# Kernel optimization log

Measured on AMD Instinct MI355X. Metric: run time of the kernel, lower is better.

## Reference

```python
import jax, jax.numpy as jnp
import numpy as np

N_QUBITS = 4
DIM = 2 ** N_QUBITS  # 16
N_PATCH = 14 * 14    # 196 patches of 2x2 on a 28x28 image
NUM_CLASSES = 10


def setup_inputs() -> dict:
    key = jax.random.key(0)
    kx, kw, kb, ku = jax.random.split(key, 4)
    B = 8192
    x = jax.random.uniform(kx, (B, 1, 28, 28), dtype=jnp.float32)
    # RandomLayer (8 random 2-qubit gates) composed into one fixed 16x16 real
    # orthogonal unitary (real because RY encoding + real-parameter gates).
    rng = np.random.default_rng(0)
    A = rng.standard_normal((DIM, DIM)).astype(np.float32)
    Q, _ = np.linalg.qr(A)
    U = jnp.asarray(Q, dtype=jnp.float32)
    W = jax.random.normal(kw, (NUM_CLASSES, N_PATCH * N_QUBITS), dtype=jnp.float32) * 0.02
    b = jax.random.normal(kb, (NUM_CLASSES,), dtype=jnp.float32) * 0.02
    return {"x": x, "U": U, "W": W, "b": b}


def _quanv_features(x, U):
    B = x.shape[0]
    # extract 2x2 patches in row-major order: data = [x[r,c], x[r,c+1], x[r+1,c], x[r+1,c+1]]
    p = x.reshape(B, 14, 2, 14, 2).transpose(0, 1, 3, 2, 4).reshape(B, N_PATCH, 4)
    half = 0.5 * p
    a = jnp.stack([jnp.cos(half), jnp.sin(half)], axis=-1)  # (B,P,4,2): RY(theta)|0>
    # product state over 4 qubits -> statevector (B,P,16), wire 0 = most significant
    state = jnp.einsum('bpi,bpj,bpk,bpl->bpijkl',
                       a[:, :, 0], a[:, :, 1], a[:, :, 2], a[:, :, 3]).reshape(B, N_PATCH, DIM)
    state = jnp.einsum('bpd,ed->bpe', state, U)  # apply random-layer unitary
    probs = state * state                          # (B,P,16), real amplitudes
    # PauliZ expectation per wire: sign (+1/-1) of each qubit bit in basis index
    bits = (jnp.arange(DIM)[:, None] >> jnp.arange(N_QUBITS - 1, -1, -1)[None, :]) & 1
    zsign = (1.0 - 2.0 * bits).astype(jnp.float32)  # (16,4)
    meas = probs @ zsign                             # (B,P,4)
    return meas.reshape(B, N_PATCH * N_QUBITS)       # patch-major, qubit-minor (matches torch.cat)


def reference(x, U, W, b):
    feat = _quanv_features(x, U)
    logits = feat @ W.T + b
    return jax.nn.log_softmax(logits, axis=-1)
```

## Files before the change

### kernel.cpp

```cpp
#include <hip/hip_runtime.h>

typedef __attribute__((ext_vector_type(8))) short short8;
typedef __attribute__((ext_vector_type(4))) float f32x4;

#define THREADS 256
#define WPB 4
#define N_PATCH 196
#define NCLS 10
#define FEAT 784
#define ROWSH 24

union I4S8 { int i[4]; short8 v; };

__global__ __launch_bounds__(THREADS, 4)
void quanv_mfma_kernel(const float* __restrict__ x,
                       const float* __restrict__ U,
                       const float* __restrict__ W,
                       const float* __restrict__ b,
                       float* __restrict__ out, int n_img)
{
    __shared__ unsigned short sB[WPB][2][64][ROWSH];

    const int t    = threadIdx.x;
    const int w    = t >> 6;
    const int lane = t & 63;
    const int img  = blockIdx.x * WPB + w;
    if (img >= n_img) return;

    const int colc = lane & 15;
    const int kb   = lane >> 4;
    const float sgn0 = (kb & 2) ? -1.f : 1.f;
    const float sgn1 = (kb & 1) ? -1.f : 1.f;

    short8 a1, a2;
    {
        const float* Urow = U + colc * 16 + (kb & 1) * 8;
        unsigned ub[8]; float uf[8];
#pragma unroll
        for (int i = 0; i < 8; ++i) { uf[i] = Urow[i]; ub[i] = __float_as_uint(uf[i]); }
        I4S8 hi, lo;
#pragma unroll
        for (int j = 0; j < 4; ++j)
            hi.i[j] = (int)__builtin_amdgcn_perm(ub[2*j+1], ub[2*j], 0x07060302u);
#pragma unroll
        for (int j = 0; j < 4; ++j) {
            unsigned lb0 = __float_as_uint(uf[2*j]   - __uint_as_float(ub[2*j]   & 0xffff0000u));
            unsigned lb1 = __float_as_uint(uf[2*j+1] - __uint_as_float(ub[2*j+1] & 0xffff0000u));
            lo.i[j] = (kb < 2) ? (int)__builtin_amdgcn_perm(lb1, lb0, 0x07060302u) : 0;
        }
        a1 = hi.v; a2 = lo.v;
    }

    const float* ximg = x + (size_t)img * FEAT;

    float acc[NCLS];
#pragma unroll
    for (int c = 0; c < NCLS; ++c) acc[c] = 0.f;

#pragma unroll 1
    for (int it = 0; it < 4; ++it) {
        asm volatile("s_waitcnt lgkmcnt(0)" ::: "memory");

        const int pm    = it * 64 + lane;
        const bool vld  = (pm < N_PATCH);
        const int  pc   = vld ? pm : N_PATCH - 1;
        const int  r    = pc / 14;
        const int  cl   = pc - r * 14;
        const float* px = ximg + r * 56 + cl * 2;
        const float2 top = *(const float2*)px;
        const float2 bot = *(const float2*)(px + 28);

        const float c0 = __cosf(0.5f * top.x), s0 = __sinf(0.5f * top.x);
        const float c1 = __cosf(0.5f * top.y), s1 = __sinf(0.5f * top.y);
        const float c2 = __cosf(0.5f * bot.x), s2 = __sinf(0.5f * bot.x);
        const float c3 = __cosf(0.5f * bot.y), s3 = __sinf(0.5f * bot.y);

        const float wm = vld ? 1.f : 0.f;
        const float p00 = wm * c0 * c1, p01 = wm * c0 * s1;
        const float p10 = wm * s0 * c1, p11 = wm * s0 * s1;
        const float q00 = c2 * c3, q01 = c2 * s3, q10 = s2 * c3, q11 = s2 * s3;
        float st[16];
        st[ 0]=p00*q00; st[ 1]=p00*q01; st[ 2]=p00*q10; st[ 3]=p00*q11;
        st[ 4]=p01*q00; st[ 5]=p01*q01; st[ 6]=p01*q10; st[ 7]=p01*q11;
        st[ 8]=p10*q00; st[ 9]=p10*q01; st[10]=p10*q10; st[11]=p10*q11;
        st[12]=p11*q00; st[13]=p11*q01; st[14]=p11*q10; st[15]=p11*q11;

        I4S8 h0, h1, l0, l1;
#pragma unroll
        for (int j = 0; j < 8; ++j) {
            const unsigned b0 = __float_as_uint(st[2*j]);
            const unsigned b1 = __float_as_uint(st[2*j+1]);
            const unsigned hp = __builtin_amdgcn_perm(b1, b0, 0x07060302u);
            const unsigned lb0 = __float_as_uint(st[2*j]   - __uint_as_float(b0 & 0xffff0000u));
            const unsigned lb1 = __float_as_uint(st[2*j+1] - __uint_as_float(b1 & 0xffff0000u));
            const unsigned lp = __builtin_amdgcn_perm(lb1, lb0, 0x07060302u);
            if (j < 4) { h0.i[j] = (int)hp; l0.i[j] = (int)lp; }
            else       { h1.i[j-4] = (int)hp; l1.i[j-4] = (int)lp; }
        }
        *(short8*)&sB[w][0][lane][0] = h0.v;
        *(short8*)&sB[w][0][lane][8] = h1.v;
        *(short8*)&sB[w][1][lane][0] = l0.v;
        *(short8*)&sB[w][1][lane][8] = l1.v;

        asm volatile("s_waitcnt lgkmcnt(0)" ::: "memory");
        __builtin_amdgcn_sched_barrier(0);

#pragma unroll
        for (int g = 0; g < 4; ++g) {
            const int q = 16 * g + colc;
            const unsigned short* src = (kb < 2) ? &sB[w][0][q][8 * (kb & 1)]
                                                 : &sB[w][1][q][8 * (kb & 1)];
            const short8 bf = *(const short8*)src;

            f32x4 amv = {0.f, 0.f, 0.f, 0.f};
            amv = __builtin_amdgcn_mfma_f32_16x16x32_bf16(a1, bf, amv, 0, 0, 0);
            amv = __builtin_amdgcn_mfma_f32_16x16x32_bf16(a2, bf, amv, 0, 0, 0);

            const float sq0 = amv[0]*amv[0], sq1 = amv[1]*amv[1];
            const float sq2 = amv[2]*amv[2], sq3 = amv[3]*amv[3];
            const float t01 = sq0 + sq1, t23 = sq2 + sq3, sall = t01 + t23;
            float m0 = sgn0 * sall;
            float m1 = sgn1 * sall;
            float m2 = t01 - t23;
            float m3 = (sq0 - sq1) + (sq2 - sq3);

            m0 += __shfl_xor(m0, 16, 64); m0 += __shfl_xor(m0, 32, 64);
            m1 += __shfl_xor(m1, 16, 64); m1 += __shfl_xor(m1, 32, 64);
            m2 += __shfl_xor(m2, 16, 64); m2 += __shfl_xor(m2, 32, 64);
            m3 += __shfl_xor(m3, 16, 64); m3 += __shfl_xor(m3, 32, 64);

            const int pg  = it * 64 + q;
            const int pcl = (pg < N_PATCH) ? pg : N_PATCH - 1;
#pragma unroll
            for (int c = 0; c < NCLS; ++c) {
                const float4 wv = *(const float4*)&W[c * FEAT + 4 * pcl];
                acc[c] = fmaf(m0, wv.x, fmaf(m1, wv.y, fmaf(m2, wv.z, fmaf(m3, wv.w, acc[c]))));
            }
        }
    }

#pragma unroll
    for (int c = 0; c < NCLS; ++c) {
        float v = acc[c];
        v += __shfl_xor(v, 1, 64);
        v += __shfl_xor(v, 2, 64);
        v += __shfl_xor(v, 4, 64);
        v += __shfl_xor(v, 8, 64);
        acc[c] = v + b[c];
    }

    float m = acc[0];
#pragma unroll
    for (int c = 1; c < NCLS; ++c) m = fmaxf(m, acc[c]);
    float ssum = 0.f;
#pragma unroll
    for (int c = 0; c < NCLS; ++c) ssum += __expf(acc[c] - m);
    const float ls = __logf(ssum);

    float v = 0.f;
#pragma unroll
    for (int c = 0; c < NCLS; ++c) if (lane == c) v = acc[c];
    if (lane < NCLS)
        out[(size_t)img * NCLS + lane] = v - m - ls;
}

extern "C" void kernel_launch(void* const* d_in, const int* in_sizes, int n_in,
                              void* d_out, int out_size, void* d_ws, size_t ws_size,
                              hipStream_t stream) {
    const float* x = (const float*)d_in[0];
    const float* U = (const float*)d_in[1];
    const float* W = (const float*)d_in[2];
    const float* b = (const float*)d_in[3];
    float* out = (float*)d_out;

    const int n_img = in_sizes[0] / FEAT;
    const int grid  = (n_img + WPB - 1) / WPB;

    quanv_mfma_kernel<<<grid, THREADS, 0, stream>>>(x, U, W, b, out, n_img);
}
```

Before: 113.9 us.

## Prefetch next patch tile, merge LDS buffers, and defer cross-group reduction

The next iteration's pixel loads are now issued before the current iteration's trig and MFMA work, which hides global load latency. The hi and lo bf16 planes share one padded LDS row per patch, and the explicit lgkmcnt waits and sched barrier are removed. Per-patch xor-16/32 shuffles of the measurements are dropped: the weighted accumulation is linear, so the cross-kb sum is done once at the end. Launch bounds now request 8 waves per SIMD, which may limit registers and cause spills.

```diff
diff --git a/kernel.cpp b/kernel.cpp
--- a/kernel.cpp
+++ b/kernel.cpp
@@ -8,18 +8,18 @@
 #define N_PATCH 196
 #define NCLS 10
 #define FEAT 784
-#define ROWSH 24
+#define ROWSH 40
 
 union I4S8 { int i[4]; short8 v; };
 
-__global__ __launch_bounds__(THREADS, 4)
+__global__ __launch_bounds__(THREADS, 8)
 void quanv_mfma_kernel(const float* __restrict__ x,
                        const float* __restrict__ U,
                        const float* __restrict__ W,
                        const float* __restrict__ b,
                        float* __restrict__ out, int n_img)
 {
-    __shared__ unsigned short sB[WPB][2][64][ROWSH];
+    __shared__ unsigned short sB[WPB][64][ROWSH];
 
     const int t    = threadIdx.x;
     const int w    = t >> 6;
@@ -57,18 +57,28 @@
 #pragma unroll
     for (int c = 0; c < NCLS; ++c) acc[c] = 0.f;
 
+    float2 top, bot;
+    {
+        const int r = lane / 14, cl = lane - r * 14;
+        const float* px = ximg + r * 56 + cl * 2;
+        top = *(const float2*)px;
+        bot = *(const float2*)(px + 28);
+    }
+
 #pragma unroll 1
     for (int it = 0; it < 4; ++it) {
-        asm volatile("s_waitcnt lgkmcnt(0)" ::: "memory");
+        float2 ntop = top, nbot = bot;
+        if (it < 3) {
+            const int pmn = (it + 1) * 64 + lane;
+            const int pcn = (pmn < N_PATCH) ? pmn : N_PATCH - 1;
+            const int r = pcn / 14, cl = pcn - r * 14;
+            const float* px = ximg + r * 56 + cl * 2;
+            ntop = *(const float2*)px;
+            nbot = *(const float2*)(px + 28);
+        }
 
-        const int pm    = it * 64 + lane;
-        const bool vld  = (pm < N_PATCH);
-        const int  pc   = vld ? pm : N_PATCH - 1;
-        const int  r    = pc / 14;
-        const int  cl   = pc - r * 14;
-        const float* px = ximg + r * 56 + cl * 2;
-        const float2 top = *(const float2*)px;
-        const float2 bot = *(const float2*)(px + 28);
+        const int pm   = it * 64 + lane;
+        const bool vld = (pm < N_PATCH);
 
         const float c0 = __cosf(0.5f * top.x), s0 = __sinf(0.5f * top.x);
         const float c1 = __cosf(0.5f * top.y), s1 = __sinf(0.5f * top.y);
@@ -97,20 +107,15 @@
             if (j < 4) { h0.i[j] = (int)hp; l0.i[j] = (int)lp; }
             else       { h1.i[j-4] = (int)hp; l1.i[j-4] = (int)lp; }
         }
-        *(short8*)&sB[w][0][lane][0] = h0.v;
-        *(short8*)&sB[w][0][lane][8] = h1.v;
-        *(short8*)&sB[w][1][lane][0] = l0.v;
-        *(short8*)&sB[w][1][lane][8] = l1.v;
-
-        asm volatile("s_waitcnt lgkmcnt(0)" ::: "memory");
-        __builtin_amdgcn_sched_barrier(0);
+        *(short8*)&sB[w][lane][ 0] = h0.v;
+        *(short8*)&sB[w][lane][ 8] = h1.v;
+        *(short8*)&sB[w][lane][16] = l0.v;
+        *(short8*)&sB[w][lane][24] = l1.v;
 
 #pragma unroll
         for (int g = 0; g < 4; ++g) {
             const int q = 16 * g + colc;
-            const unsigned short* src = (kb < 2) ? &sB[w][0][q][8 * (kb & 1)]
-                                                 : &sB[w][1][q][8 * (kb & 1)];
-            const short8 bf = *(const short8*)src;
+            const short8 bf = *(const short8*)&sB[w][q][8 * kb];
 
             f32x4 amv = {0.f, 0.f, 0.f, 0.f};
             amv = __builtin_amdgcn_mfma_f32_16x16x32_bf16(a1, bf, amv, 0, 0, 0);
@@ -119,15 +124,10 @@
             const float sq0 = amv[0]*amv[0], sq1 = amv[1]*amv[1];
             const float sq2 = amv[2]*amv[2], sq3 = amv[3]*amv[3];
             const float t01 = sq0 + sq1, t23 = sq2 + sq3, sall = t01 + t23;
-            float m0 = sgn0 * sall;
-            float m1 = sgn1 * sall;
-            float m2 = t01 - t23;
-            float m3 = (sq0 - sq1) + (sq2 - sq3);
-
-            m0 += __shfl_xor(m0, 16, 64); m0 += __shfl_xor(m0, 32, 64);
-            m1 += __shfl_xor(m1, 16, 64); m1 += __shfl_xor(m1, 32, 64);
-            m2 += __shfl_xor(m2, 16, 64); m2 += __shfl_xor(m2, 32, 64);
-            m3 += __shfl_xor(m3, 16, 64); m3 += __shfl_xor(m3, 32, 64);
+            const float m0 = sgn0 * sall;
+            const float m1 = sgn1 * sall;
+            const float m2 = t01 - t23;
+            const float m3 = (sq0 - sq1) + (sq2 - sq3);
 
             const int pg  = it * 64 + q;
             const int pcl = (pg < N_PATCH) ? pg : N_PATCH - 1;
@@ -137,15 +137,19 @@
                 acc[c] = fmaf(m0, wv.x, fmaf(m1, wv.y, fmaf(m2, wv.z, fmaf(m3, wv.w, acc[c]))));
             }
         }
+
+        top = ntop; bot = nbot;
     }
 
 #pragma unroll
     for (int c = 0; c < NCLS; ++c) {
         float v = acc[c];
-        v += __shfl_xor(v, 1, 64);
-        v += __shfl_xor(v, 2, 64);
-        v += __shfl_xor(v, 4, 64);
-        v += __shfl_xor(v, 8, 64);
+        v += __shfl_xor(v,  1, 64);
+        v += __shfl_xor(v,  2, 64);
+        v += __shfl_xor(v,  4, 64);
+        v += __shfl_xor(v,  8, 64);
+        v += __shfl_xor(v, 16, 64);
+        v += __shfl_xor(v, 32, 64);
         acc[c] = v + b[c];
     }
 
```

Result: slower. 120.7 us (+5.9%).
